# Kernel optimization log

Measured on AMD Instinct MI355X. Metric: run time of the kernel, lower is better.

Reference implementation:

```python
import jax, jax.numpy as jnp
import numpy as np

NEG = -9e15

def setup_inputs() -> dict:
    key = jax.random.key(0)
    k1, k2, k3, k4, k5 = jax.random.split(key, 5)
    N, Fin, Fout = 8192, 256, 128
    h = jax.random.normal(k1, (N, Fin), dtype=jnp.float32)
    adj = jax.random.randint(k2, (N, N), 0, 2, dtype=jnp.int32)
    # Parameters (xavier_uniform with gain=1.414 for a1/a2; kaiming-like for W is fine as random init)
    lim_w = float(np.sqrt(6.0 / (Fin + Fout)))
    W = jax.random.uniform(k3, (Fout, Fin), dtype=jnp.float32, minval=-lim_w, maxval=lim_w)
    lim_a = float(1.414 * np.sqrt(6.0 / (Fout + 1)))
    a1 = jax.random.uniform(k4, (Fout, 1), dtype=jnp.float32, minval=-lim_a, maxval=lim_a)
    a2 = jax.random.uniform(k5, (Fout, 1), dtype=jnp.float32, minval=-lim_a, maxval=lim_a)
    return {"h": h, "adj": adj, "W": W, "a1": a1, "a2": a2}

def reference(h, adj, W, a1, a2):
    Wh = h @ W.T                                   # [N, Fout]
    s1 = (Wh @ a1)                                 # [N, 1]
    s2 = (Wh @ a2)                                 # [N, 1]
    e = jax.nn.leaky_relu(s1 + s2.T, 0.2)          # [N, N]
    att = jnp.where(adj > 0, e, jnp.float32(NEG))
    att = jax.nn.softmax(att, axis=1)
    h_prime = att @ Wh                             # [N, Fout]
    return jax.nn.elu(h_prime)
```

## Files before the change

kernel.cpp:

```cpp
#include <hip/hip_runtime.h>
#include <cstdint>
#include <cstddef>


#define N_NODES 8192
#define FIN 256
#define FOUT 128
#define MT 16
#define KC 256
#define JS 2
#define JW (N_NODES / JS)
#define NCHS (JW / KC)

typedef __attribute__((ext_vector_type(8))) short bf16x8;
typedef __attribute__((ext_vector_type(4))) float f32x4;
typedef __attribute__((ext_vector_type(4))) int i32x4;
typedef __attribute__((ext_vector_type(2))) unsigned int u32x2;

__device__ __forceinline__ float bf2f(unsigned short u) {
    union { unsigned int i; float f; } v; v.i = ((unsigned int)u) << 16; return v.f;
}
__device__ __forceinline__ unsigned short f2bf(float f) {
    union { float f; unsigned int i; } v; v.f = f;
    unsigned int r = (v.i + 0x7FFFu + ((v.i >> 16) & 1u)) >> 16;
    return (unsigned short)r;
}

__global__ __launch_bounds__(256) void wh_kernel(const float* __restrict__ h,
                                                 const float* __restrict__ W,
                                                 unsigned short* __restrict__ whT) {
    __shared__ float hT[64][FIN + 5];
    const int t = threadIdx.x;
    const int i0 = blockIdx.x * 64;
    const int f0 = blockIdx.y * 32;
#pragma unroll
    for (int c = 0; c < 16; ++c) {
        int chunk = c * 256 + t;
        int row = chunk >> 6, col = (chunk & 63) * 4;
        f32x4 v = *(const f32x4*)&h[(size_t)(i0 + row) * FIN + col];
        hT[row][col] = v[0]; hT[row][col + 1] = v[1];
        hT[row][col + 2] = v[2]; hT[row][col + 3] = v[3];
    }
    __syncthreads();
    const int lane = t & 63;
    const int fb = __builtin_amdgcn_readfirstlane(f0 + (t >> 6) * 8);
    const float* w0 = W + (size_t)fb * FIN;
    float acc[8] = {0.f, 0.f, 0.f, 0.f, 0.f, 0.f, 0.f, 0.f};
    for (int k = 0; k < FIN; k += 4) {
        float h0 = hT[lane][k],     h1 = hT[lane][k + 1];
        float h2 = hT[lane][k + 2], h3 = hT[lane][k + 3];
#pragma unroll
        for (int c = 0; c < 8; ++c) {
            const float* wr = w0 + c * FIN;
            acc[c] += h0 * wr[k] + h1 * wr[k + 1] + h2 * wr[k + 2] + h3 * wr[k + 3];
        }
    }
#pragma unroll
    for (int c = 0; c < 8; ++c)
        whT[(size_t)(fb + c) * N_NODES + i0 + lane] = f2bf(acc[c]);
}

__global__ __launch_bounds__(256) void s_kernel(const unsigned short* __restrict__ whT,
                                                const float* __restrict__ a1,
                                                const float* __restrict__ a2,
                                                float* __restrict__ s1,
                                                float* __restrict__ s2) {
    __shared__ float p1[4][64], p2[4][64];
    const int t = threadIdx.x;
    const int l = t & 63;
    const int g = t >> 6;
    const int i = blockIdx.x * 64 + l;
    float acc1 = 0.f, acc2 = 0.f;
#pragma unroll
    for (int fo = 0; fo < 32; ++fo) {
        int f = g * 32 + fo;
        float v = bf2f(whT[(size_t)f * N_NODES + i]);
        acc1 += v * a1[f];
        acc2 += v * a2[f];
    }
    p1[g][l] = acc1; p2[g][l] = acc2;
    __syncthreads();
    if (g == 0) {
        s1[i] = p1[0][l] + p1[1][l] + p1[2][l] + p1[3][l];
        s2[i] = p2[0][l] + p2[1][l] + p2[2][l] + p2[3][l];
    }
}

__global__ __launch_bounds__(256) void gat_kernel(const int* __restrict__ adj,
                                                  const unsigned short* __restrict__ whT,
                                                  const float* __restrict__ s1,
                                                  const float* __restrict__ s2,
                                                  float* __restrict__ num0,
                                                  float* __restrict__ num1,
                                                  float* __restrict__ den0,
                                                  float* __restrict__ den1) {
    __shared__ __align__(16) unsigned short sP[MT][KC + 8];
    __shared__ float sDen[MT];
    __shared__ float sS1[MT];
    const int t = threadIdx.x;
    const int slice = blockIdx.x & 1;
    const int i0 = (blockIdx.x >> 1) * MT;
    const int jb = slice * JW;
    float* __restrict__ num = slice ? num1 : num0;
    float* __restrict__ den = slice ? den1 : den0;
    if (t < MT) { sDen[t] = 0.f; sS1[t] = s1[i0 + t]; }
    __syncthreads();

    const int ii = t >> 4;
    const int s  = t & 15;
    const int lane = t & 63;
    const int quad = lane >> 4;
    const int sl = lane & 15;
    const int wv = t >> 6;
    const int* adjRow = adj + (size_t)(i0 + ii) * N_NODES;
    const float s1i = sS1[ii];

    f32x4 acc[2];
    acc[0] = (f32x4){0.f, 0.f, 0.f, 0.f};
    acc[1] = (f32x4){0.f, 0.f, 0.f, 0.f};

    i32x4 aj[4]; f32x4 sv[4];
#pragma unroll
    for (int q = 0; q < 4; ++q) {
        int col = jb + q * 64 + s * 4;
        aj[q] = *(const i32x4*)&adjRow[col];
        sv[q] = *(const f32x4*)&s2[col];
    }

    for (int ch = 0; ch < NCHS; ++ch) {
        const int j0 = jb + ch * KC;
        float part = 0.f;
#pragma unroll
        for (int q = 0; q < 4; ++q) {
            float p[4];
#pragma unroll
            for (int r = 0; r < 4; ++r) {
                float x = s1i + sv[q][r];
                x = fmaxf(x, 0.2f * x);
                x = fminf(x, 60.f);
                float e = __expf(x);
                p[r] = (aj[q][r] > 0) ? e : 0.f;
                part += p[r];
            }
            u32x2 pk;
            pk.x = (unsigned)f2bf(p[0]) | ((unsigned)f2bf(p[1]) << 16);
            pk.y = (unsigned)f2bf(p[2]) | ((unsigned)f2bf(p[3]) << 16);
            *(u32x2*)&sP[ii][q * 64 + s * 4] = pk;
        }
        if (ch + 1 < NCHS) {
            int jn = j0 + KC;
#pragma unroll
            for (int q = 0; q < 4; ++q) {
                int col = jn + q * 64 + s * 4;
                aj[q] = *(const i32x4*)&adjRow[col];
                sv[q] = *(const f32x4*)&s2[col];
            }
        }
        part += __shfl_xor(part, 1);
        part += __shfl_xor(part, 2);
        part += __shfl_xor(part, 4);
        part += __shfl_xor(part, 8);
        if (s == 0) sDen[ii] += part;
        __syncthreads();
#pragma unroll
        for (int kq = 0; kq < KC / 32; ++kq) {
            bf16x8 af = *(const bf16x8*)&sP[sl][kq * 32 + quad * 8];
#pragma unroll
            for (int nn = 0; nn < 2; ++nn) {
                int f = wv * 32 + nn * 16 + sl;
                bf16x8 bf = *(const bf16x8*)&whT[(size_t)f * N_NODES + j0 + kq * 32 + quad * 8];
                acc[nn] = __builtin_amdgcn_mfma_f32_16x16x32_bf16(af, bf, acc[nn], 0, 0, 0);
            }
        }
        __syncthreads();
    }
    if (t < MT) den[i0 + t] = sDen[t];
#pragma unroll
    for (int nn = 0; nn < 2; ++nn) {
#pragma unroll
        for (int r = 0; r < 4; ++r) {
            int row = quad * 4 + r;
            num[(size_t)(i0 + row) * FOUT + wv * 32 + nn * 16 + sl] = acc[nn][r];
        }
    }
}

__global__ __launch_bounds__(256) void fin_kernel(float* __restrict__ out,
                                                  const float* __restrict__ num1,
                                                  const float* __restrict__ den0,
                                                  const float* __restrict__ den1) {
    const int idx = blockIdx.x * 256 + threadIdx.x;
    const int i = idx >> 7;
    float numv = out[idx] + num1[idx];
    float denv = fmaxf(den0[i] + den1[i], 1e-30f);
    float v = numv / denv;
    out[idx] = (v > 0.f) ? v : expm1f(v);
}

extern "C" void kernel_launch(void* const* d_in, const int* in_sizes, int n_in,
                              void* d_out, int out_size, void* d_ws, size_t ws_size,
                              hipStream_t stream) {
    const float* h   = (const float*)d_in[0];
    const int*   adj = (const int*)d_in[1];
    const float* W   = (const float*)d_in[2];
    const float* a1  = (const float*)d_in[3];
    const float* a2  = (const float*)d_in[4];

    unsigned short* whT = (unsigned short*)d_ws;
    float* s1   = (float*)d_in[0];
    float* s2   = s1 + N_NODES;
    float* num1 = s2 + N_NODES;
    float* den0 = num1 + (size_t)N_NODES * FOUT;
    float* den1 = den0 + N_NODES;
    float* num0 = (float*)d_out;

    wh_kernel<<<dim3(N_NODES / 64, FOUT / 32), 256, 0, stream>>>(h, W, whT);
    s_kernel<<<dim3(N_NODES / 64), 256, 0, stream>>>(whT, a1, a2, s1, s2);
    gat_kernel<<<dim3((N_NODES / MT) * JS), 256, 0, stream>>>(adj, whT, s1, s2,
                                                              num0, num1, den0, den1);
    fin_kernel<<<dim3(N_NODES * FOUT / 256), 256, 0, stream>>>(num0, num1, den0, den1);
}
```

Before: 464.5 us.

## Process 32 rows per block with MFMA-fragment Wh layout and exp2

Doubles rows per block so each Wh B-fragment loaded from global memory feeds two MFMAs, halving Wh traffic per output row. Wh is stored in a blocked layout matching the 16x16x32 fragment so each lane does one contiguous 16-byte load. The softmax exponent uses exp2 with log2(e) folded into s1/s2, and the clamp at 60 is dropped. This halves the number of blocks, which may reduce occupancy, and raises register pressure. Without the clamp, large scores could overflow to inf.

```diff
diff --git a/kernel.cpp b/kernel.cpp
--- a/kernel.cpp
+++ b/kernel.cpp
@@ -2,15 +2,15 @@
 #include <cstdint>
 #include <cstddef>
 
-
 #define N_NODES 8192
 #define FIN 256
 #define FOUT 128
-#define MT 16
+#define MT 32
 #define KC 256
 #define JS 2
 #define JW (N_NODES / JS)
 #define NCHS (JW / KC)
+#define LOG2E 1.4426950408889634f
 
 typedef __attribute__((ext_vector_type(8))) short bf16x8;
 typedef __attribute__((ext_vector_type(4))) float f32x4;
@@ -25,10 +25,18 @@
     unsigned int r = (v.i + 0x7FFFu + ((v.i >> 16) & 1u)) >> 16;
     return (unsigned short)r;
 }
+__device__ __forceinline__ unsigned int pack_bf16(float a, float b) {
+    return (unsigned)f2bf(a) | ((unsigned)f2bf(b) << 16);
+}
+
+__device__ __forceinline__ size_t whb_idx(int j, int f) {
+    return ((size_t)((j >> 5) * 8 + (f >> 4)) << 9) + (((j >> 3) & 3) << 7)
+         + ((f & 15) << 3) + (j & 7);
+}
 
 __global__ __launch_bounds__(256) void wh_kernel(const float* __restrict__ h,
                                                  const float* __restrict__ W,
-                                                 unsigned short* __restrict__ whT) {
+                                                 unsigned short* __restrict__ whB) {
     __shared__ float hT[64][FIN + 5];
     const int t = threadIdx.x;
     const int i0 = blockIdx.x * 64;
@@ -43,8 +51,8 @@
     }
     __syncthreads();
     const int lane = t & 63;
-    const int fb = __builtin_amdgcn_readfirstlane(f0 + (t >> 6) * 8);
-    const float* w0 = W + (size_t)fb * FIN;
+    const int fb8 = __builtin_amdgcn_readfirstlane(f0 + (t >> 6) * 8);
+    const float* w0 = W + (size_t)fb8 * FIN;
     float acc[8] = {0.f, 0.f, 0.f, 0.f, 0.f, 0.f, 0.f, 0.f};
     for (int k = 0; k < FIN; k += 4) {
         float h0 = hT[lane][k],     h1 = hT[lane][k + 1];
@@ -55,12 +63,13 @@
             acc[c] += h0 * wr[k] + h1 * wr[k + 1] + h2 * wr[k + 2] + h3 * wr[k + 3];
         }
     }
+    const int i = i0 + lane;
 #pragma unroll
     for (int c = 0; c < 8; ++c)
-        whT[(size_t)(fb + c) * N_NODES + i0 + lane] = f2bf(acc[c]);
-}
-
-__global__ __launch_bounds__(256) void s_kernel(const unsigned short* __restrict__ whT,
+        whB[whb_idx(i, fb8 + c)] = f2bf(acc[c]);
+}
+
+__global__ __launch_bounds__(256) void s_kernel(const unsigned short* __restrict__ whB,
                                                 const float* __restrict__ a1,
                                                 const float* __restrict__ a2,
                                                 float* __restrict__ s1,
@@ -72,22 +81,25 @@
     const int i = blockIdx.x * 64 + l;
     float acc1 = 0.f, acc2 = 0.f;
 #pragma unroll
-    for (int fo = 0; fo < 32; ++fo) {
-        int f = g * 32 + fo;
-        float v = bf2f(whT[(size_t)f * N_NODES + i]);
-        acc1 += v * a1[f];
-        acc2 += v * a2[f];
+    for (int fb = g * 2; fb < g * 2 + 2; ++fb) {
+#pragma unroll
+        for (int sl = 0; sl < 16; ++sl) {
+            int f = fb * 16 + sl;
+            float v = bf2f(whB[whb_idx(i, f)]);
+            acc1 += v * a1[f];
+            acc2 += v * a2[f];
+        }
     }
     p1[g][l] = acc1; p2[g][l] = acc2;
     __syncthreads();
     if (g == 0) {
-        s1[i] = p1[0][l] + p1[1][l] + p1[2][l] + p1[3][l];
-        s2[i] = p2[0][l] + p2[1][l] + p2[2][l] + p2[3][l];
+        s1[i] = (p1[0][l] + p1[1][l] + p1[2][l] + p1[3][l]) * LOG2E;
+        s2[i] = (p2[0][l] + p2[1][l] + p2[2][l] + p2[3][l]) * LOG2E;
     }
 }
 
 __global__ __launch_bounds__(256) void gat_kernel(const int* __restrict__ adj,
-                                                  const unsigned short* __restrict__ whT,
+                                                  const unsigned short* __restrict__ whB,
                                                   const float* __restrict__ s1,
                                                   const float* __restrict__ s2,
                                                   float* __restrict__ num0,
@@ -101,86 +113,101 @@
     const int slice = blockIdx.x & 1;
     const int i0 = (blockIdx.x >> 1) * MT;
     const int jb = slice * JW;
+    const int kb0 = slice * (JW / 32);
     float* __restrict__ num = slice ? num1 : num0;
     float* __restrict__ den = slice ? den1 : den0;
     if (t < MT) { sDen[t] = 0.f; sS1[t] = s1[i0 + t]; }
     __syncthreads();
 
-    const int ii = t >> 4;
+    const int r0 = t >> 4;
     const int s  = t & 15;
     const int lane = t & 63;
     const int quad = lane >> 4;
     const int sl = lane & 15;
     const int wv = t >> 6;
-    const int* adjRow = adj + (size_t)(i0 + ii) * N_NODES;
-    const float s1i = sS1[ii];
-
-    f32x4 acc[2];
-    acc[0] = (f32x4){0.f, 0.f, 0.f, 0.f};
-    acc[1] = (f32x4){0.f, 0.f, 0.f, 0.f};
-
-    i32x4 aj[4]; f32x4 sv[4];
+    const int* adjRow0 = adj + (size_t)(i0 + r0) * N_NODES;
+    const int* adjRow1 = adjRow0 + (size_t)16 * N_NODES;
+    const float s1a = sS1[r0];
+    const float s1b = sS1[r0 + 16];
+
+    f32x4 acc00 = {0.f,0.f,0.f,0.f}, acc01 = {0.f,0.f,0.f,0.f};
+    f32x4 acc10 = {0.f,0.f,0.f,0.f}, acc11 = {0.f,0.f,0.f,0.f};
+
+    i32x4 aj0[4], aj1[4]; f32x4 sv[4];
 #pragma unroll
     for (int q = 0; q < 4; ++q) {
         int col = jb + q * 64 + s * 4;
-        aj[q] = *(const i32x4*)&adjRow[col];
-        sv[q] = *(const f32x4*)&s2[col];
+        aj0[q] = *(const i32x4*)&adjRow0[col];
+        aj1[q] = *(const i32x4*)&adjRow1[col];
+        sv[q]  = *(const f32x4*)&s2[col];
     }
 
     for (int ch = 0; ch < NCHS; ++ch) {
-        const int j0 = jb + ch * KC;
-        float part = 0.f;
+        float part0 = 0.f, part1 = 0.f;
 #pragma unroll
         for (int q = 0; q < 4; ++q) {
-            float p[4];
+            float p0[4], p1v[4];
 #pragma unroll
             for (int r = 0; r < 4; ++r) {
-                float x = s1i + sv[q][r];
-                x = fmaxf(x, 0.2f * x);
-                x = fminf(x, 60.f);
-                float e = __expf(x);
-                p[r] = (aj[q][r] > 0) ? e : 0.f;
-                part += p[r];
+                float y0 = s1a + sv[q][r];
+                float y1 = s1b + sv[q][r];
+                y0 = fmaxf(y0, 0.2f * y0);
+                y1 = fmaxf(y1, 0.2f * y1);
+                float e0 = __builtin_amdgcn_exp2f(y0);
+                float e1 = __builtin_amdgcn_exp2f(y1);
+                p0[r]  = (aj0[q][r] > 0) ? e0 : 0.f;
+                p1v[r] = (aj1[q][r] > 0) ? e1 : 0.f;
+                part0 += p0[r];
+                part1 += p1v[r];
             }
-            u32x2 pk;
-            pk.x = (unsigned)f2bf(p[0]) | ((unsigned)f2bf(p[1]) << 16);
-            pk.y = (unsigned)f2bf(p[2]) | ((unsigned)f2bf(p[3]) << 16);
-            *(u32x2*)&sP[ii][q * 64 + s * 4] = pk;
+            u32x2 pk0, pk1;
+            pk0.x = pack_bf16(p0[0], p0[1]);   pk0.y = pack_bf16(p0[2], p0[3]);
+            pk1.x = pack_bf16(p1v[0], p1v[1]); pk1.y = pack_bf16(p1v[2], p1v[3]);
+            *(u32x2*)&sP[r0][q * 64 + s * 4] = pk0;
+            *(u32x2*)&sP[r0 + 16][q * 64 + s * 4] = pk1;
         }
         if (ch + 1 < NCHS) {
-            int jn = j0 + KC;
+            int jn = jb + (ch + 1) * KC;
 #pragma unroll
             for (int q = 0; q < 4; ++q) {
                 int col = jn + q * 64 + s * 4;
-                aj[q] = *(const i32x4*)&adjRow[col];
-                sv[q] = *(const f32x4*)&s2[col];
+                aj0[q] = *(const i32x4*)&adjRow0[col];
+                aj1[q] = *(const i32x4*)&adjRow1[col];
+                sv[q]  = *(const f32x4*)&s2[col];
             }
         }
-        part += __shfl_xor(part, 1);
-        part += __shfl_xor(part, 2);
-        part += __shfl_xor(part, 4);
-        part += __shfl_xor(part, 8);
-        if (s == 0) sDen[ii] += part;
+        part0 += __shfl_xor(part0, 1); part1 += __shfl_xor(part1, 1);
+        part0 += __shfl_xor(part0, 2); part1 += __shfl_xor(part1, 2);
+        part0 += __shfl_xor(part0, 4); part1 += __shfl_xor(part1, 4);
+        part0 += __shfl_xor(part0, 8); part1 += __shfl_xor(part1, 8);
+        if (s == 0) { sDen[r0] += part0; sDen[r0 + 16] += part1; }
         __syncthreads();
 #pragma unroll
         for (int kq = 0; kq < KC / 32; ++kq) {
-            bf16x8 af = *(const bf16x8*)&sP[sl][kq * 32 + quad * 8];
-#pragma unroll
-            for (int nn = 0; nn < 2; ++nn) {
-                int f = wv * 32 + nn * 16 + sl;
-                bf16x8 bf = *(const bf16x8*)&whT[(size_t)f * N_NODES + j0 + kq * 32 + quad * 8];
-                acc[nn] = __builtin_amdgcn_mfma_f32_16x16x32_bf16(af, bf, acc[nn], 0, 0, 0);
+            bf16x8 a0  = *(const bf16x8*)&sP[sl][kq * 32 + quad * 8];
+            bf16x8 a1f = *(const bf16x8*)&sP[16 + sl][kq * 32 + quad * 8];
+            int kb = kb0 + ch * (KC / 32) + kq;
+            const unsigned short* t0 = whB + ((size_t)(kb * 8 + wv * 2) << 9) + lane * 8;
+            bf16x8 b0 = *(const bf16x8*)t0;
+            bf16x8 b1 = *(const bf16x8*)(t0 + 512);
+            acc00 = __builtin_amdgcn_mfma_f32_16x16x32_bf16(a0,  b0, acc00, 0, 0, 0);
+            acc01 = __builtin_amdgcn_mfma_f32_16x16x32_bf16(a0,  b1, acc01, 0, 0, 0);
+            acc10 = __builtin_amdgcn_mfma_f32_16x16x32_bf16(a1f, b0, acc10, 0, 0, 0);
+            acc11 = __builtin_amdgcn_mfma_f32_16x16x32_bf16(a1f, b1, acc11, 0, 0, 0);
+        }
+        __syncthreads();
+    }
+    if (t < MT) den[i0 + t] = sDen[t];
+#pragma unroll
+    for (int m = 0; m < 2; ++m) {
+#pragma unroll
+        for (int nn = 0; nn < 2; ++nn) {
+            f32x4 a = (m == 0) ? (nn == 0 ? acc00 : acc01) : (nn == 0 ? acc10 : acc11);
+#pragma unroll
+            for (int r = 0; r < 4; ++r) {
+                int row = m * 16 + quad * 4 + r;
+                num[(size_t)(i0 + row) * FOUT + wv * 32 + nn * 16 + sl] = a[r];
             }
-        }
-        __syncthreads();
-    }
-    if (t < MT) den[i0 + t] = sDen[t];
-#pragma unroll
-    for (int nn = 0; nn < 2; ++nn) {
-#pragma unroll
-        for (int r = 0; r < 4; ++r) {
-            int row = quad * 4 + r;
-            num[(size_t)(i0 + row) * FOUT + wv * 32 + nn * 16 + sl] = acc[nn][r];
         }
     }
 }
@@ -206,7 +233,7 @@
     const float* a1  = (const float*)d_in[3];
     const float* a2  = (const float*)d_in[4];
 
-    unsigned short* whT = (unsigned short*)d_ws;
+    unsigned short* whB = (unsigned short*)d_ws;
     float* s1   = (float*)d_in[0];
     float* s2   = s1 + N_NODES;
     float* num1 = s2 + N_NODES;
@@ -214,9 +241,9 @@
     float* den1 = den0 + N_NODES;
     float* num0 = (float*)d_out;
 
-    wh_kernel<<<dim3(N_NODES / 64, FOUT / 32), 256, 0, stream>>>(h, W, whT);
-    s_kernel<<<dim3(N_NODES / 64), 256, 0, stream>>>(whT, a1, a2, s1, s2);
-    gat_kernel<<<dim3((N_NODES / MT) * JS), 256, 0, stream>>>(adj, whT, s1, s2,
+    wh_kernel<<<dim3(N_NODES / 64, FOUT / 32), 256, 0, stream>>>(h, W, whB);
+    s_kernel<<<dim3(N_NODES / 64), 256, 0, stream>>>(whB, a1, a2, s1, s2);
+    gat_kernel<<<dim3((N_NODES / MT) * JS), 256, 0, stream>>>(adj, whB, s1, s2,
                                                               num0, num1, den0, den1);
     fin_kernel<<<dim3(N_NODES * FOUT / 256), 256, 0, stream>>>(num0, num1, den0, den1);
 }
```

After: 435.5 us. 1.07x faster.
